# Kernel tuning notes

Measured on AMD Instinct MI355X. Metric: run time of the kernel, lower is better.

## Reference

```python
import jax, jax.numpy as jnp
import numpy as np

N_FFT = 1024
HOP = 256
N_MELS = 128
SR = 16000
EPS = 1e-6
S = 0.025
ALPHA = 0.98
DELTA = 2.0
R = 0.5


def make_mel_fb():
    # Faithful port of F2M._init_buffers (onesided=True)
    n_freq = N_FFT // 2 + 1
    f_max = SR // 2
    m_min = 0.0
    m_max = 2595.0 * np.log10(1.0 + f_max / 700.0)
    m_pts = np.linspace(m_min, m_max, N_MELS + 2)
    f_pts = 700.0 * (10.0 ** (m_pts / 2595.0) - 1.0)
    bins = np.floor((n_freq - 1) * 2 * f_pts / SR).astype(np.int64)
    fb = np.zeros((n_freq, N_MELS), dtype=np.float32)
    for m in range(1, N_MELS + 1):
        a, b, c = int(bins[m - 1]), int(bins[m]), int(bins[m + 1])
        if a != b:
            fb[a:b, m - 1] = (np.arange(a, b) - a) / (b - a)
        if b != c:
            fb[b:c, m - 1] = (c - np.arange(b, c)) / (c - b)
    return jnp.asarray(fb)


def setup_inputs() -> dict:
    key = jax.random.key(0)
    x = jax.random.normal(key, (32, 160000), dtype=jnp.float32)
    return {"x": x, "fb": make_mel_fb()}


def reference(x, fb):
    # torch.stft with center=True (default), rectangular window (window=None)
    pad = N_FFT // 2
    xp = jnp.pad(x, ((0, 0), (pad, pad)), mode="reflect")
    n_frames = (xp.shape[1] - N_FFT) // HOP + 1
    idx = jnp.arange(n_frames)[:, None] * HOP + jnp.arange(N_FFT)[None, :]
    frames = xp[:, idx]                       # [B, T, n_fft]
    spec = jnp.abs(jnp.fft.rfft(frames, axis=-1))   # magnitude, [B, T, F]
    mel = jnp.einsum("btf,fm->btm", spec, fb)       # [B, T, M]

    # PCEN EMA smoother: M_0 = x_0, M_t = (1-s) M_{t-1} + s x_t
    def step(m_prev, frame):
        m = (1.0 - S) * m_prev + S * frame
        return m, m

    x0 = mel[:, 0, :]                               # [B, M]
    _, ms = jax.lax.scan(step, x0, jnp.swapaxes(mel[:, 1:, :], 0, 1))
    M = jnp.concatenate([x0[:, None, :], jnp.swapaxes(ms, 0, 1)], axis=1)

    out = (mel / (M + EPS) ** ALPHA + DELTA) ** R - DELTA ** R
    return out
```

## Files before the change

kernel.cpp:

```cpp
#include <hip/hip_runtime.h>
#include <math.h>

#define NMELS   128
#define NFRAMES 626
#define NPAIRS  313
#define NBATCH  32
#define LSAMP   160000
#define NFREQ   513
#define PPB     4
#define NBLK    ((NPAIRS + PPB - 1) / PPB)
#define NCHUNK  NBLK

struct Bins { int v[NMELS + 2]; };

__device__ __forceinline__ int refl(int i) {
    if (i < 0) i = -i;
    else if (i >= LSAMP) i = 2 * LSAMP - 2 - i;
    return i;
}

__device__ __forceinline__ int band_of(int i, int r) {
    switch (i) {
        case 0:  return r;
        case 1:  return 127 - r;
        case 2:  return 32 + r;
        default: return 95 - r;
    }
}

__device__ __forceinline__ float2 cadd(float2 a, float2 b){return make_float2(a.x+b.x, a.y+b.y);}
__device__ __forceinline__ float2 csub(float2 a, float2 b){return make_float2(a.x-b.x, a.y-b.y);}
__device__ __forceinline__ float2 cmul(float2 a, float2 b){
    return make_float2(fmaf(a.x,b.x,-a.y*b.y), fmaf(a.x,b.y,a.y*b.x));
}
__device__ __forceinline__ float2 cmulnegi(float2 a){return make_float2(a.y, -a.x);}

__device__ __forceinline__ void dft16(float2* z) {
    const float2 W1 = make_float2( 0.92387953251f, -0.38268343236f);
    const float2 W2 = make_float2( 0.70710678119f, -0.70710678119f);
    const float2 W3 = make_float2( 0.38268343236f, -0.92387953251f);
    const float2 W6 = make_float2(-0.70710678119f, -0.70710678119f);
    const float2 W9 = make_float2(-0.92387953251f,  0.38268343236f);
    float2 g[16];
    #pragma unroll
    for (int q = 0; q < 4; q++) {
        float2 t0=z[q], t1=z[4+q], t2=z[8+q], t3=z[12+q];
        float2 A=cadd(t0,t2), B=csub(t0,t2), C=cadd(t1,t3), D=csub(t1,t3);
        g[q]    = cadd(A,C);
        g[4+q]  = make_float2(B.x + D.y, B.y - D.x);
        g[8+q]  = csub(A,C);
        g[12+q] = make_float2(B.x - D.y, B.y + D.x);
    }
    g[4+1] =cmul(g[4+1], W1); g[4+2] =cmul(g[4+2], W2); g[4+3] =cmul(g[4+3], W3);
    g[8+1] =cmul(g[8+1], W2); g[8+2] =cmulnegi(g[8+2]); g[8+3] =cmul(g[8+3], W6);
    g[12+1]=cmul(g[12+1],W3); g[12+2]=cmul(g[12+2],W6);  g[12+3]=cmul(g[12+3],W9);
    #pragma unroll
    for (int r = 0; r < 4; r++) {
        float2 t0=g[4*r], t1=g[4*r+1], t2=g[4*r+2], t3=g[4*r+3];
        float2 A=cadd(t0,t2), B=csub(t0,t2), C=cadd(t1,t3), D=csub(t1,t3);
        z[r]    = cadd(A,C);
        z[r+4]  = make_float2(B.x + D.y, B.y - D.x);
        z[r+8]  = csub(A,C);
        z[r+12] = make_float2(B.x - D.y, B.y + D.x);
    }
}

__global__ __launch_bounds__(256, 4)
void fft_mel_kernel(const float* __restrict__ x, float* __restrict__ mel,
                    float* __restrict__ S, Bins bins) {
    __shared__ float2 wbuf[PPB][1088];

    const int tid = threadIdx.x;
    const int w   = tid >> 6;
    const int u   = tid & 63;
    const int P   = blockIdx.x;
    const int b   = blockIdx.y;
    const int p   = P * PPB + w;

    float acc[4];

    if (p < NPAIRS) {
        float2* buf  = wbuf[w];
        float*  raw  = (float*)&wbuf[w][0];
        float*  spec = (float*)&wbuf[w][0];

        const float* xb = x + (size_t)b * LSAMP;
        const int base = 512 * p - 512;
        if (p != 0 && p != NPAIRS - 1) {
            const float* xs = xb + base;
            #pragma unroll
            for (int j = 0; j < 5; j++) {
                const int i = 256 * j + 4 * u;
                float4 v = *reinterpret_cast<const float4*>(xs + i);
                *reinterpret_cast<float4*>(raw + i) = v;
            }
        } else {
            #pragma unroll
            for (int j = 0; j < 20; j++) {
                const int i = 64 * j + u;
                raw[i] = xb[refl(base + i)];
            }
        }

        float2 z[16];

        #pragma unroll
        for (int a = 0; a < 16; a++)
            z[a] = make_float2(raw[64*a + u], raw[64*a + u + 256]);
        dft16(z);
        {
            float s, c; __sincosf(-(float)M_PI * (float)u * (1.0f/512.0f), &s, &c);
            float2 w1 = make_float2(c, s), wk = w1;
            #pragma unroll
            for (int k = 1; k < 16; k++) { z[k] = cmul(z[k], wk); wk = cmul(wk, w1); }
        }
        #pragma unroll
        for (int k = 0; k < 16; k++) buf[17*u + k] = z[k];

        const int k1 = u >> 2, bp = u & 3;
        #pragma unroll
        for (int a = 0; a < 16; a++) z[a] = buf[68*a + 17*bp + k1];
        dft16(z);
        {
            float s, c; __sincosf(-(float)M_PI * (float)bp * (1.0f/32.0f), &s, &c);
            float2 w1 = make_float2(c, s), wk = w1;
            #pragma unroll
            for (int k = 1; k < 16; k++) { z[k] = cmul(z[k], wk); wk = cmul(wk, w1); }
        }
        #pragma unroll
        for (int k = 0; k < 16; k++) buf[68*k + 17*bp + k1] = z[k];

        #pragma unroll
        for (int j = 0; j < 4; j++) {
            const int c = 64*j + u;
            const int kk1 = c & 15, k2a = c >> 4;
            #pragma unroll
            for (int bq = 0; bq < 4; bq++) z[4*j + bq] = buf[68*k2a + 17*bq + kk1];
        }
        #pragma unroll
        for (int j = 0; j < 4; j++) {
            const int kbase = u + 64*j;
            float2 t0=z[4*j], t1=z[4*j+1], t2=z[4*j+2], t3=z[4*j+3];
            float2 A=cadd(t0,t2), B=csub(t0,t2), C=cadd(t1,t3), D=csub(t1,t3);
            buf[kbase]       = cadd(A,C);
            buf[kbase + 256] = make_float2(B.x + D.y, B.y - D.x);
            buf[kbase + 512] = csub(A,C);
            buf[kbase + 768] = make_float2(B.x - D.y, B.y + D.x);
        }

        float m0[9], m1[9];
        #pragma unroll
        for (int j = 0; j < 9; j++) {
            const int k = 64*j + u;
            if (k <= 512) {
                const int nk = (1024 - k) & 1023;
                float2 Zk = buf[k], Zn = buf[nk];
                float ar = Zk.x + Zn.x, ai = Zk.y - Zn.y;
                float br = Zk.y + Zn.y, bi = Zn.x - Zk.x;
                m0[j] = 0.5f * sqrtf(ar*ar + ai*ai);
                m1[j] = 0.5f * sqrtf(br*br + bi*bi);
            }
        }
        #pragma unroll
        for (int j = 0; j < 9; j++) {
            const int k = 64*j + u;
            if (k <= 512) { spec[k] = m0[j]; spec[NFREQ + k] = m1[j]; }
        }

        const int r = u & 31, pf = u >> 5;
        const float* sp = spec + pf * NFREQ;
        #pragma unroll
        for (int i = 0; i < 4; i++) {
            const int mm = band_of(i, r);
            const int a = bins.v[mm], bb = bins.v[mm+1], c = bins.v[mm+2];
            float a0 = 0.f;
            if (bb > a) {
                float s0 = 0.f, s1 = 0.f;
                int f = a;
                for (; f + 1 < bb; f += 2) {
                    s0 = fmaf(sp[f],     (float)(f     - a), s0);
                    s1 = fmaf(sp[f + 1], (float)(f + 1 - a), s1);
                }
                if (f < bb) s0 = fmaf(sp[f], (float)(f - a), s0);
                a0 += (s0 + s1) * __builtin_amdgcn_rcpf((float)(bb - a));
            }
            if (c > bb) {
                float s0 = 0.f, s1 = 0.f;
                int f = bb;
                for (; f + 1 < c; f += 2) {
                    s0 = fmaf(sp[f],     (float)(c - f),     s0);
                    s1 = fmaf(sp[f + 1], (float)(c - f - 1), s1);
                }
                if (f < c) s0 = fmaf(sp[f], (float)(c - f), s0);
                a0 += (s0 + s1) * __builtin_amdgcn_rcpf((float)(c - bb));
            }
            acc[i] = a0;
            mel[((size_t)b * NFRAMES + 2*p + pf) * NMELS + mm] = a0;
        }
    }
    __syncthreads();

    float* melst = (float*)&wbuf[0][544];
    if (p < NPAIRS) {
        const int r = u & 31, pf = u >> 5;
        const int fl = 2*w + pf;
        #pragma unroll
        for (int i = 0; i < 4; i++) melst[fl*NMELS + band_of(i, r)] = acc[i];
    }
    __syncthreads();

    if (tid < NMELS) {
        const int t0 = P * 8;
        const int nf = (NFRAMES - t0 < 8) ? NFRAMES - t0 : 8;
        float s = 0.f;
        for (int f = 0; f < nf; f++) {
            float v = melst[f*NMELS + tid];
            s = (t0 + f == 0) ? v : fmaf(0.975f, s, 0.025f * v);
        }
        S[((size_t)b * NCHUNK + P) * NMELS + tid] = s;
    }
}

__global__ __launch_bounds__(256)
void pcen_scan(const float* __restrict__ S, float* __restrict__ Mstart) {
    const int idx = blockIdx.x * 256 + threadIdx.x;
    const int m = idx & 127;
    const int b = idx >> 7;
    if (b >= NBATCH) return;

    float D8; { float d = 0.975f; d *= d; d *= d; d *= d; D8 = d; }

    const size_t base = (size_t)b * NCHUNK * NMELS + m;
    float M = 0.f;
    #pragma unroll 8
    for (int c = 0; c < NCHUNK; c++) {
        Mstart[base + (size_t)c * NMELS] = M;
        M = fmaf(D8, M, S[base + (size_t)c * NMELS]);
    }
}

__global__ __launch_bounds__(128)
void pcen_out(const float* __restrict__ mel, const float* __restrict__ Mstart,
              float* __restrict__ out) {
    const int m = threadIdx.x;
    const int c = blockIdx.x;
    const int b = blockIdx.y;

    float M = Mstart[((size_t)b * NCHUNK + c) * NMELS + m];

    const int t0 = c * 8;
    const int tend = (t0 + 8 < NFRAMES) ? t0 + 8 : NFRAMES;
    const float* mp = mel + (size_t)b * NFRAMES * NMELS + m;
    float*       op = out + (size_t)b * NFRAMES * NMELS + m;
    #pragma unroll 8
    for (int t = t0; t < tend; t++) {
        float v = mp[(size_t)t * NMELS];
        M = (t == 0) ? v : fmaf(0.975f, M, 0.025f * v);
        float inv = __builtin_amdgcn_exp2f(-0.98f * __builtin_amdgcn_logf(M + 1e-6f));
        op[(size_t)t * NMELS] = sqrtf(fmaf(v, inv, 2.0f)) - 1.41421356237f;
    }
}

extern "C" void kernel_launch(void* const* d_in, const int* in_sizes, int n_in,
                              void* d_out, int out_size, void* d_ws, size_t ws_size,
                              hipStream_t stream) {
    const float* x  = (const float*)d_in[0];
    float* out = (float*)d_out;

    float* mel    = (float*)d_ws;
    float* S      = mel + (size_t)NBATCH * NFRAMES * NMELS;
    float* Mstart = S   + (size_t)NBATCH * NCHUNK * NMELS;

    Bins bins;
    {
        const double m_max = 2595.0 * log10(1.0 + 8000.0 / 700.0);
        const double step  = m_max / 129.0;
        for (int i = 0; i < NMELS + 2; i++) {
            double mv = (i == NMELS + 1) ? m_max : (double)i * step;
            double f  = 700.0 * (pow(10.0, mv / 2595.0) - 1.0);
            bins.v[i] = (int)floor((double)(NFREQ - 1) * 2.0 * f / 16000.0);
        }
    }

    dim3 grid1(NBLK, NBATCH);
    fft_mel_kernel<<<grid1, 256, 0, stream>>>(x, mel, S, bins);

    pcen_scan<<<(NBATCH * NMELS + 255) / 256, 256, 0, stream>>>(S, Mstart);

    dim3 grid3(NCHUNK, NBATCH);
    pcen_out<<<grid3, 128, 0, stream>>>(mel, Mstart, out);
}
```

Before: 109.3 us.

## Fold PCEN chunk scan into output kernel via weighted sum of chunk partials

Removes the separate serial pcen_scan kernel and its Mstart buffer. Each pcen_out block now computes its starting EMA state directly as a decayed weighted sum of all preceding chunk partials, using four accumulators to split the dependency chain. This saves a kernel launch and the 79-step serial scan. In exchange the work grows quadratically, since later chunks read up to 78 partials each, and the float summation order changes.

```diff
diff --git a/kernel.cpp b/kernel.cpp
--- a/kernel.cpp
+++ b/kernel.cpp
@@ -221,32 +221,32 @@
     }
 }
 
-__global__ __launch_bounds__(256)
-void pcen_scan(const float* __restrict__ S, float* __restrict__ Mstart) {
-    const int idx = blockIdx.x * 256 + threadIdx.x;
-    const int m = idx & 127;
-    const int b = idx >> 7;
-    if (b >= NBATCH) return;
-
-    float D8; { float d = 0.975f; d *= d; d *= d; d *= d; D8 = d; }
-
-    const size_t base = (size_t)b * NCHUNK * NMELS + m;
-    float M = 0.f;
-    #pragma unroll 8
-    for (int c = 0; c < NCHUNK; c++) {
-        Mstart[base + (size_t)c * NMELS] = M;
-        M = fmaf(D8, M, S[base + (size_t)c * NMELS]);
-    }
-}
-
 __global__ __launch_bounds__(128)
-void pcen_out(const float* __restrict__ mel, const float* __restrict__ Mstart,
+void pcen_out(const float* __restrict__ mel, const float* __restrict__ S,
               float* __restrict__ out) {
     const int m = threadIdx.x;
     const int c = blockIdx.x;
     const int b = blockIdx.y;
 
-    float M = Mstart[((size_t)b * NCHUNK + c) * NMELS + m];
+    float D8; { float d = 0.975f; d *= d; d *= d; d *= d; D8 = d; }
+
+    float M = 0.f;
+    if (c > 0) {
+        const float* Sp = S + (size_t)b * NCHUNK * NMELS + m;
+        float D32 = D8 * D8; D32 *= D32;
+        float a0 = 0.f, a1 = 0.f, a2 = 0.f, a3 = 0.f;
+        float w0 = 1.f, w1 = D8, w2 = D8 * D8, w3 = w2 * D8;
+        int j = c - 1;
+        for (; j >= 3; j -= 4) {
+            a0 = fmaf(w0, Sp[(size_t)j       * NMELS], a0);
+            a1 = fmaf(w1, Sp[(size_t)(j - 1) * NMELS], a1);
+            a2 = fmaf(w2, Sp[(size_t)(j - 2) * NMELS], a2);
+            a3 = fmaf(w3, Sp[(size_t)(j - 3) * NMELS], a3);
+            w0 *= D32; w1 *= D32; w2 *= D32; w3 *= D32;
+        }
+        for (; j >= 0; j--) { a0 = fmaf(w0, Sp[(size_t)j * NMELS], a0); w0 *= D8; }
+        M = (a0 + a1) + (a2 + a3);
+    }
 
     const int t0 = c * 8;
     const int tend = (t0 + 8 < NFRAMES) ? t0 + 8 : NFRAMES;
@@ -267,9 +267,8 @@
     const float* x  = (const float*)d_in[0];
     float* out = (float*)d_out;
 
-    float* mel    = (float*)d_ws;
-    float* S      = mel + (size_t)NBATCH * NFRAMES * NMELS;
-    float* Mstart = S   + (size_t)NBATCH * NCHUNK * NMELS;
+    float* mel = (float*)d_ws;
+    float* S   = mel + (size_t)NBATCH * NFRAMES * NMELS;
 
     Bins bins;
     {
@@ -285,8 +284,6 @@
     dim3 grid1(NBLK, NBATCH);
     fft_mel_kernel<<<grid1, 256, 0, stream>>>(x, mel, S, bins);
 
-    pcen_scan<<<(NBATCH * NMELS + 255) / 256, 256, 0, stream>>>(S, Mstart);
-
-    dim3 grid3(NCHUNK, NBATCH);
-    pcen_out<<<grid3, 128, 0, stream>>>(mel, Mstart, out);
-}
+    dim3 grid2(NCHUNK, NBATCH);
+    pcen_out<<<grid2, 128, 0, stream>>>(mel, S, out);
+}
```

Measured after the change: 105.5 us, median of 2. 1.04x faster.
